# Kernel optimization log

Hardware: AMD Instinct MI355X
Metric: run time of the kernel (lower is better)

The kernel has to match this reference:

```python
import jax, jax.numpy as jnp
import numpy as np

TIME = 10  # interpolation factor, hardcoded in the torch module


def _interpolation(poly, time=TIME):
    # poly: [B, M, 2] -> [B, M*time, 2]
    poly_roll = jnp.roll(poly, shift=1, axis=1)
    step = jnp.arange(time, dtype=poly.dtype) / time  # [time]
    # interp[b, m, t, c] = poly[b,m,c]*step[t] + roll[b,m,c]*(1-step[t])
    interp = (poly[:, :, None, :] * step[None, None, :, None]
              + poly_roll[:, :, None, :] * (1.0 - step)[None, None, :, None])
    B, M = poly.shape[0], poly.shape[1]
    return interp.reshape(B, M * time, 2)


def _compute_distance(pred_poly, gt_poly):
    # pred: [B, N, 2], gt: [B, G, 2] -> sq dist [B, G, N]
    diff = pred_poly[:, None, :, :] - gt_poly[:, :, None, :]
    return jnp.sum(diff * diff, axis=3)


def setup_inputs() -> dict:
    key = jax.random.key(0)
    k1, k2, k3 = jax.random.split(key, 3)
    B, N, M = 1024, 128, 128
    return {
        "ini_pred_poly": jax.random.normal(k1, (B, N, 2), dtype=jnp.float32),
        "pred_polys_": jax.random.normal(k2, (B, N, 2), dtype=jnp.float32),
        "gt_polys": jax.random.normal(k3, (B, M, 2), dtype=jnp.float32),
        "keyPointsMask": jnp.ones((B, M), dtype=jnp.float32),
    }


def reference(ini_pred_poly, pred_polys_, gt_polys, keyPointsMask):
    # ---- lossPred2NearestGt ----
    gt_interp = _interpolation(gt_polys)                     # [B, M*T, 2]
    dist_pg = _compute_distance(ini_pred_poly, gt_interp)    # [B, M*T, N]
    index_gt = jnp.argmin(dist_pg, axis=1)                   # [B, N]
    nearest_gt = jnp.take_along_axis(gt_interp, index_gt[:, :, None], axis=1)  # [B, N, 2]
    loss_pred2gt = jnp.mean(jnp.abs(pred_polys_ - nearest_gt))  # l1, mean reduction

    # ---- lossGt2NearestPred ----
    dist_gp = _compute_distance(ini_pred_poly, gt_polys)     # [B, M, N]
    index_pred = jnp.argmin(dist_gp, axis=2)                 # [B, M]
    nearest_pred = jnp.take_along_axis(pred_polys_, index_pred[:, :, None], axis=1)  # [B, M, 2]
    loss_gt2pred = jnp.abs(nearest_pred - gt_polys)          # [B, M, 2], reduction='none'

    mask = keyPointsMask[:, :, None] * jnp.ones((1, 1, 2), dtype=keyPointsMask.dtype)  # [B, M, 2]
    loss_set2set = jnp.sum(loss_gt2pred * mask) / (jnp.sum(mask) + 1.0) + loss_pred2gt
    return loss_set2set / 2.0
```

## Files before the change

### kernel.cpp

```cpp
#include <hip/hip_runtime.h>

constexpr int Bn = 1024;
constexpr int Nn = 128;
constexpr int Mn = 128;


__global__ __launch_bounds__(256) void dm_main(
    const float2* __restrict__ ini,
    const float2* __restrict__ pred,
    const float2* __restrict__ gt,
    const float*  __restrict__ kpm,
    float4* __restrict__ part)
{
    __shared__ float4 s_segA[Mn];
    __shared__ float2 s_segB[Mn];
    __shared__ float2 s_ini[Nn];
    __shared__ float2 s_pred[Nn];
    __shared__ float2 s_gt[Mn];
    __shared__ float  s_red[3][4];

    const int b   = blockIdx.x;
    const int tid = threadIdx.x;

    if (tid < Mn) {
        const float2 cur = gt[b*Mn + tid];
        const float2 prv = gt[b*Mn + ((tid + Mn - 1) & (Mn - 1))];
        const float ex = cur.x - prv.x, ey = cur.y - prv.y;
        const float ee = fmaxf(fmaf(ex, ex, ey*ey), 1e-30f);
        const float nr = -10.0f * __builtin_amdgcn_rcpf(ee);
        s_segA[tid] = make_float4(prv.x, prv.y, ex, ey);
        s_segB[tid] = make_float2(ee, nr);
        s_gt[tid]   = cur;
        s_ini[tid]  = ini[b*Nn + tid];
        s_pred[tid] = pred[b*Nn + tid];
    }
    __syncthreads();

    const int lane_s = tid & 1;
    const int n      = tid >> 1;
    const int base   = lane_s * 64;

    const float2 p = s_ini[n];
    float best = 3.4e38f; int bm = 0; float bs = 0.f;
    #pragma unroll 8
    for (int i = 0; i < 64; ++i) {
        const int m = base + i;
        const float4 A  = s_segA[m];
        const float2 Bv = s_segB[m];
        const float fx = A.x - p.x, fy = A.y - p.y;
        const float fe = fmaf(fx, A.z, fy*A.w);
        const float ff = fmaf(fx, fx, fy*fy);
        float tv = fe * Bv.y;
        tv = fminf(fmaxf(rintf(tv), 0.f), 9.f);
        const float sp = tv * 0.1f;
        const float d  = fmaf(sp, fmaf(sp, Bv.x, fe + fe), ff);
        if (d < best) { best = d; bm = m; bs = sp; }
    }
    {
        const float od = __shfl_xor(best, 1);
        const int   om = __shfl_xor(bm, 1);
        const float os = __shfl_xor(bs, 1);
        if (od < best || (od == best && om < bm)) { best = od; bm = om; bs = os; }
    }
    float sum_p2g = 0.f;
    if (lane_s == 0) {
        const float4 A = s_segA[bm];
        const float ngx = fmaf(bs, A.z, A.x);
        const float ngy = fmaf(bs, A.w, A.y);
        const float2 pr = s_pred[n];
        sum_p2g = fabsf(pr.x - ngx) + fabsf(pr.y - ngy);
    }

    const float2 g = s_gt[n];
    float best2 = 3.4e38f; int ni = 0;
    #pragma unroll 8
    for (int i = 0; i < 64; ++i) {
        const int j = base + i;
        const float2 q = s_ini[j];
        const float dx = q.x - g.x, dy = q.y - g.y;
        const float d = fmaf(dx, dx, dy*dy);
        if (d < best2) { best2 = d; ni = j; }
    }
    {
        const float od = __shfl_xor(best2, 1);
        const int   oi = __shfl_xor(ni, 1);
        if (od < best2 || (od == best2 && oi < ni)) { best2 = od; ni = oi; }
    }
    float sum_g2p = 0.f, sum_m = 0.f;
    if (lane_s == 0) {
        const float  w   = kpm[b*Mn + n];
        const float2 np_ = s_pred[ni];
        sum_g2p = w * (fabsf(np_.x - g.x) + fabsf(np_.y - g.y));
        sum_m   = 2.0f * w;
    }

    #pragma unroll
    for (int off = 32; off > 0; off >>= 1) {
        sum_p2g += __shfl_down(sum_p2g, off);
        sum_g2p += __shfl_down(sum_g2p, off);
        sum_m   += __shfl_down(sum_m,   off);
    }
    const int wv = tid >> 6;
    if ((tid & 63) == 0) { s_red[0][wv] = sum_p2g; s_red[1][wv] = sum_g2p; s_red[2][wv] = sum_m; }
    __syncthreads();
    if (tid == 0) {
        part[b] = make_float4(s_red[0][0] + s_red[0][1] + s_red[0][2] + s_red[0][3],
                              s_red[1][0] + s_red[1][1] + s_red[1][2] + s_red[1][3],
                              s_red[2][0] + s_red[2][1] + s_red[2][2] + s_red[2][3], 0.f);
    }
}

__global__ __launch_bounds__(1024) void dm_final(const float4* __restrict__ part,
                                                 float* __restrict__ out)
{
    __shared__ float s_red[3][16];
    const int tid = threadIdx.x;
    const float4 v = part[tid];
    float a = v.x, c = v.y, m = v.z;
    #pragma unroll
    for (int off = 32; off > 0; off >>= 1) {
        a += __shfl_down(a, off); c += __shfl_down(c, off); m += __shfl_down(m, off);
    }
    const int wv = tid >> 6;
    if ((tid & 63) == 0) { s_red[0][wv] = a; s_red[1][wv] = c; s_red[2][wv] = m; }
    __syncthreads();
    if (tid == 0) {
        float A = 0.f, C = 0.f, M = 0.f;
        #pragma unroll
        for (int i = 0; i < 16; ++i) { A += s_red[0][i]; C += s_red[1][i]; M += s_red[2][i]; }
        out[0] = (C / (M + 1.0f) + A * (1.0f / 262144.0f)) * 0.5f;
    }
}

extern "C" void kernel_launch(void* const* d_in, const int* in_sizes, int n_in,
                              void* d_out, int out_size, void* d_ws, size_t ws_size,
                              hipStream_t stream)
{
    const float2* ini  = (const float2*)d_in[0];
    const float2* pred = (const float2*)d_in[1];
    const float2* gt   = (const float2*)d_in[2];
    const float*  kpm  = (const float*)d_in[3];
    float*  out  = (float*)d_out;
    float4* part = (float4*)d_ws;

    dm_main<<<Bn, 256, 0, stream>>>(ini, pred, gt, kpm, part);
    dm_final<<<1, 1024, 0, stream>>>(part, out);
}
```

Before: 73.31 us.

## Split each batch across two blocks and pack argmin into sortable keys

```diff
diff --git a/kernel.cpp b/kernel.cpp
--- a/kernel.cpp
+++ b/kernel.cpp
@@ -19,7 +19,8 @@
     __shared__ float2 s_gt[Mn];
     __shared__ float  s_red[3][4];
 
-    const int b   = blockIdx.x;
+    const int b   = blockIdx.x >> 1;
+    const int h   = blockIdx.x & 1;
     const int tid = threadIdx.x;
 
     if (tid < Mn) {
@@ -27,69 +28,68 @@
         const float2 prv = gt[b*Mn + ((tid + Mn - 1) & (Mn - 1))];
         const float ex = cur.x - prv.x, ey = cur.y - prv.y;
         const float ee = fmaxf(fmaf(ex, ex, ey*ey), 1e-30f);
-        const float nr = -10.0f * __builtin_amdgcn_rcpf(ee);
         s_segA[tid] = make_float4(prv.x, prv.y, ex, ey);
-        s_segB[tid] = make_float2(ee, nr);
+        s_segB[tid] = make_float2(ee, -10.0f * __builtin_amdgcn_rcpf(ee));
         s_gt[tid]   = cur;
         s_ini[tid]  = ini[b*Nn + tid];
         s_pred[tid] = pred[b*Nn + tid];
     }
     __syncthreads();
 
-    const int lane_s = tid & 1;
-    const int n      = tid >> 1;
-    const int base   = lane_s * 64;
+    const int p    = tid >> 2;
+    const int q    = tid & 3;
+    const int n    = h*64 + p;
+    const int base = q*32;
 
-    const float2 p = s_ini[n];
-    float best = 3.4e38f; int bm = 0; float bs = 0.f;
+    const float2 P = s_ini[n];
+    unsigned bestA = 0xFFFFFFFFu;
     #pragma unroll 8
-    for (int i = 0; i < 64; ++i) {
+    for (int i = 0; i < 32; ++i) {
         const int m = base + i;
         const float4 A  = s_segA[m];
         const float2 Bv = s_segB[m];
-        const float fx = A.x - p.x, fy = A.y - p.y;
+        const float fx = A.x - P.x, fy = A.y - P.y;
         const float fe = fmaf(fx, A.z, fy*A.w);
         const float ff = fmaf(fx, fx, fy*fy);
-        float tv = fe * Bv.y;
-        tv = fminf(fmaxf(rintf(tv), 0.f), 9.f);
-        const float sp = tv * 0.1f;
-        const float d  = fmaf(sp, fmaf(sp, Bv.x, fe + fe), ff);
-        if (d < best) { best = d; bm = m; bs = sp; }
+        const float sp = 0.1f * __builtin_amdgcn_fmed3f(rintf(fe*Bv.y), 0.f, 9.f);
+        const float d  = fmaxf(fmaf(sp, fmaf(sp, Bv.x, fe + fe), ff), 0.f);
+        bestA = min(bestA, (__float_as_uint(d) & 0xFFFFFF80u) | (unsigned)m);
     }
-    {
-        const float od = __shfl_xor(best, 1);
-        const int   om = __shfl_xor(bm, 1);
-        const float os = __shfl_xor(bs, 1);
-        if (od < best || (od == best && om < bm)) { best = od; bm = om; bs = os; }
-    }
+    bestA = min(bestA, (unsigned)__shfl_xor((int)bestA, 1));
+    bestA = min(bestA, (unsigned)__shfl_xor((int)bestA, 2));
+
     float sum_p2g = 0.f;
-    if (lane_s == 0) {
-        const float4 A = s_segA[bm];
-        const float ngx = fmaf(bs, A.z, A.x);
-        const float ngy = fmaf(bs, A.w, A.y);
+    if (q == 0) {
+        const int bm = bestA & 127;
+        const float4 A  = s_segA[bm];
+        const float2 Bv = s_segB[bm];
+        const float fx = A.x - P.x, fy = A.y - P.y;
+        const float fe = fmaf(fx, A.z, fy*A.w);
+        const float sp = 0.1f * __builtin_amdgcn_fmed3f(rintf(fe*Bv.y), 0.f, 9.f);
+        const float ngx = fmaf(sp, A.z, A.x);
+        const float ngy = fmaf(sp, A.w, A.y);
         const float2 pr = s_pred[n];
         sum_p2g = fabsf(pr.x - ngx) + fabsf(pr.y - ngy);
     }
 
     const float2 g = s_gt[n];
-    float best2 = 3.4e38f; int ni = 0;
+    unsigned bestB = 0xFFFFFFFFu;
     #pragma unroll 8
-    for (int i = 0; i < 64; ++i) {
+    for (int i = 0; i < 32; ++i) {
         const int j = base + i;
-        const float2 q = s_ini[j];
-        const float dx = q.x - g.x, dy = q.y - g.y;
-        const float d = fmaf(dx, dx, dy*dy);
-        if (d < best2) { best2 = d; ni = j; }
+        const float2 Qp = s_ini[j];
+        const float dx = Qp.x - g.x, dy = Qp.y - g.y;
+        const float d  = fmaf(dx, dx, dy*dy);
+        bestB = min(bestB, (__float_as_uint(d) & 0xFFFFFF80u) | (unsigned)j);
     }
-    {
-        const float od = __shfl_xor(best2, 1);
-        const int   oi = __shfl_xor(ni, 1);
-        if (od < best2 || (od == best2 && oi < ni)) { best2 = od; ni = oi; }
-    }
+    bestB = min(bestB, (unsigned)__shfl_xor((int)bestB, 1));
+    bestB = min(bestB, (unsigned)__shfl_xor((int)bestB, 2));
+
     float sum_g2p = 0.f, sum_m = 0.f;
-    if (lane_s == 0) {
-        const float  w   = kpm[b*Mn + n];
-        const float2 np_ = s_pred[ni];
+    if (q == 0) {
+        const int   ni_ = bestB & 127;
+        const float w   = kpm[b*Mn + n];
+        const float2 np_ = s_pred[ni_];
         sum_g2p = w * (fabsf(np_.x - g.x) + fabsf(np_.y - g.y));
         sum_m   = 2.0f * w;
     }
@@ -104,9 +104,10 @@
     if ((tid & 63) == 0) { s_red[0][wv] = sum_p2g; s_red[1][wv] = sum_g2p; s_red[2][wv] = sum_m; }
     __syncthreads();
     if (tid == 0) {
-        part[b] = make_float4(s_red[0][0] + s_red[0][1] + s_red[0][2] + s_red[0][3],
-                              s_red[1][0] + s_red[1][1] + s_red[1][2] + s_red[1][3],
-                              s_red[2][0] + s_red[2][1] + s_red[2][2] + s_red[2][3], 0.f);
+        part[blockIdx.x] = make_float4(
+            s_red[0][0] + s_red[0][1] + s_red[0][2] + s_red[0][3],
+            s_red[1][0] + s_red[1][1] + s_red[1][2] + s_red[1][3],
+            s_red[2][0] + s_red[2][1] + s_red[2][2] + s_red[2][3], 0.f);
     }
 }
 
@@ -115,8 +116,9 @@
 {
     __shared__ float s_red[3][16];
     const int tid = threadIdx.x;
-    const float4 v = part[tid];
-    float a = v.x, c = v.y, m = v.z;
+    const float4 v0 = part[tid];
+    const float4 v1 = part[tid + 1024];
+    float a = v0.x + v1.x, c = v0.y + v1.y, m = v0.z + v1.z;
     #pragma unroll
     for (int off = 32; off > 0; off >>= 1) {
         a += __shfl_down(a, off); c += __shfl_down(c, off); m += __shfl_down(m, off);
@@ -143,6 +145,6 @@
     float*  out  = (float*)d_out;
     float4* part = (float4*)d_ws;
 
-    dm_main<<<Bn, 256, 0, stream>>>(ini, pred, gt, kpm, part);
+    dm_main<<<2*Bn, 256, 0, stream>>>(ini, pred, gt, kpm, part);
     dm_final<<<1, 1024, 0, stream>>>(part, out);
 }
```

Measured after the change: 80.02 us. +9.1%, slower.

## Precompute segment table in separate kernel and use packed argmin keys

Applied to the files above, without the earlier changes.

```diff
diff --git a/kernel.cpp b/kernel.cpp
--- a/kernel.cpp
+++ b/kernel.cpp
@@ -1,99 +1,75 @@
 #include <hip/hip_runtime.h>
 
 constexpr int Bn = 1024;
-constexpr int Nn = 128;
 constexpr int Mn = 128;
 
 
-__global__ __launch_bounds__(256) void dm_main(
+__global__ __launch_bounds__(256) void dm_pre(
+    const float2* __restrict__ ini,
+    const float2* __restrict__ gt,
+    float4* __restrict__ seg)
+{
+    const int idx = blockIdx.x * 256 + threadIdx.x;
+    const int b = idx >> 7, m = idx & 127;
+    const float2 cur = gt[idx];
+    const float2 prv = gt[(b << 7) | ((m + 127) & 127)];
+    const float2 ii  = ini[idx];
+    const float ex = cur.x - prv.x, ey = cur.y - prv.y;
+    const float ee = fmaxf(fmaf(ex, ex, ey * ey), 1e-30f);
+    const float nr = -10.0f * __builtin_amdgcn_rcpf(ee);
+    seg[2*idx]     = make_float4(prv.x, prv.y, ex, ey);
+    seg[2*idx + 1] = make_float4(ee, nr, ii.x, ii.y);
+}
+
+__global__ __launch_bounds__(128) void dm_main(
     const float2* __restrict__ ini,
     const float2* __restrict__ pred,
     const float2* __restrict__ gt,
     const float*  __restrict__ kpm,
+    const float4* __restrict__ seg,
     float4* __restrict__ part)
 {
-    __shared__ float4 s_segA[Mn];
-    __shared__ float2 s_segB[Mn];
-    __shared__ float2 s_ini[Nn];
-    __shared__ float2 s_pred[Nn];
-    __shared__ float2 s_gt[Mn];
-    __shared__ float  s_red[3][4];
+    const int b    = blockIdx.x;
+    const int tid  = threadIdx.x;
+    const int base = b * (2 * Mn);
 
-    const int b   = blockIdx.x;
-    const int tid = threadIdx.x;
+    const float2 P = ini[b*Mn + tid];
+    const float2 g = gt [b*Mn + tid];
 
-    if (tid < Mn) {
-        const float2 cur = gt[b*Mn + tid];
-        const float2 prv = gt[b*Mn + ((tid + Mn - 1) & (Mn - 1))];
-        const float ex = cur.x - prv.x, ey = cur.y - prv.y;
-        const float ee = fmaxf(fmaf(ex, ex, ey*ey), 1e-30f);
-        const float nr = -10.0f * __builtin_amdgcn_rcpf(ee);
-        s_segA[tid] = make_float4(prv.x, prv.y, ex, ey);
-        s_segB[tid] = make_float2(ee, nr);
-        s_gt[tid]   = cur;
-        s_ini[tid]  = ini[b*Nn + tid];
-        s_pred[tid] = pred[b*Nn + tid];
-    }
-    __syncthreads();
-
-    const int lane_s = tid & 1;
-    const int n      = tid >> 1;
-    const int base   = lane_s * 64;
-
-    const float2 p = s_ini[n];
-    float best = 3.4e38f; int bm = 0; float bs = 0.f;
+    unsigned bestA = 0xFFFFFFFFu, bestB = 0xFFFFFFFFu;
     #pragma unroll 8
-    for (int i = 0; i < 64; ++i) {
-        const int m = base + i;
-        const float4 A  = s_segA[m];
-        const float2 Bv = s_segB[m];
-        const float fx = A.x - p.x, fy = A.y - p.y;
-        const float fe = fmaf(fx, A.z, fy*A.w);
+    for (int m = 0; m < Mn; ++m) {
+        const float4 A1 = seg[base + 2*m];
+        const float4 A2 = seg[base + 2*m + 1];
+        const float fx = A1.x - P.x, fy = A1.y - P.y;
+        const float fe = fmaf(fx, A1.z, fy*A1.w);
         const float ff = fmaf(fx, fx, fy*fy);
-        float tv = fe * Bv.y;
-        tv = fminf(fmaxf(rintf(tv), 0.f), 9.f);
-        const float sp = tv * 0.1f;
-        const float d  = fmaf(sp, fmaf(sp, Bv.x, fe + fe), ff);
-        if (d < best) { best = d; bm = m; bs = sp; }
-    }
-    {
-        const float od = __shfl_xor(best, 1);
-        const int   om = __shfl_xor(bm, 1);
-        const float os = __shfl_xor(bs, 1);
-        if (od < best || (od == best && om < bm)) { best = od; bm = om; bs = os; }
-    }
-    float sum_p2g = 0.f;
-    if (lane_s == 0) {
-        const float4 A = s_segA[bm];
-        const float ngx = fmaf(bs, A.z, A.x);
-        const float ngy = fmaf(bs, A.w, A.y);
-        const float2 pr = s_pred[n];
-        sum_p2g = fabsf(pr.x - ngx) + fabsf(pr.y - ngy);
+        const float sp = 0.1f * __builtin_amdgcn_fmed3f(rintf(fe*A2.y), 0.f, 9.f);
+        const float d  = fmaxf(fmaf(sp, fmaf(sp, A2.x, fe + fe), ff), 0.f);
+        bestA = min(bestA, (__float_as_uint(d) & 0xFFFFFF80u) | (unsigned)m);
+        const float dx = A2.z - g.x, dy = A2.w - g.y;
+        const float d2 = fmaf(dx, dx, dy*dy);
+        bestB = min(bestB, (__float_as_uint(d2) & 0xFFFFFF80u) | (unsigned)m);
     }
 
-    const float2 g = s_gt[n];
-    float best2 = 3.4e38f; int ni = 0;
-    #pragma unroll 8
-    for (int i = 0; i < 64; ++i) {
-        const int j = base + i;
-        const float2 q = s_ini[j];
-        const float dx = q.x - g.x, dy = q.y - g.y;
-        const float d = fmaf(dx, dx, dy*dy);
-        if (d < best2) { best2 = d; ni = j; }
-    }
-    {
-        const float od = __shfl_xor(best2, 1);
-        const int   oi = __shfl_xor(ni, 1);
-        if (od < best2 || (od == best2 && oi < ni)) { best2 = od; ni = oi; }
-    }
-    float sum_g2p = 0.f, sum_m = 0.f;
-    if (lane_s == 0) {
-        const float  w   = kpm[b*Mn + n];
-        const float2 np_ = s_pred[ni];
-        sum_g2p = w * (fabsf(np_.x - g.x) + fabsf(np_.y - g.y));
-        sum_m   = 2.0f * w;
-    }
+    const int bm = bestA & 127;
+    const float4 R1 = seg[base + 2*bm];
+    const float4 R2 = seg[base + 2*bm + 1];
+    const float fx = R1.x - P.x, fy = R1.y - P.y;
+    const float fe = fmaf(fx, R1.z, fy*R1.w);
+    const float sp = 0.1f * __builtin_amdgcn_fmed3f(rintf(fe*R2.y), 0.f, 9.f);
+    const float ngx = fmaf(sp, R1.z, R1.x);
+    const float ngy = fmaf(sp, R1.w, R1.y);
+    const float2 pr = pred[b*Mn + tid];
+    float sum_p2g = fabsf(pr.x - ngx) + fabsf(pr.y - ngy);
 
+    const int   ni_ = bestB & 127;
+    const float2 np_ = pred[b*Mn + ni_];
+    const float  w   = kpm[b*Mn + tid];
+    float sum_g2p = w * (fabsf(np_.x - g.x) + fabsf(np_.y - g.y));
+    float sum_m   = 2.0f * w;
+
+    __shared__ float s_red[3][2];
     #pragma unroll
     for (int off = 32; off > 0; off >>= 1) {
         sum_p2g += __shfl_down(sum_p2g, off);
@@ -104,9 +80,9 @@
     if ((tid & 63) == 0) { s_red[0][wv] = sum_p2g; s_red[1][wv] = sum_g2p; s_red[2][wv] = sum_m; }
     __syncthreads();
     if (tid == 0) {
-        part[b] = make_float4(s_red[0][0] + s_red[0][1] + s_red[0][2] + s_red[0][3],
-                              s_red[1][0] + s_red[1][1] + s_red[1][2] + s_red[1][3],
-                              s_red[2][0] + s_red[2][1] + s_red[2][2] + s_red[2][3], 0.f);
+        part[b] = make_float4(s_red[0][0] + s_red[0][1],
+                              s_red[1][0] + s_red[1][1],
+                              s_red[2][0] + s_red[2][1], 0.f);
     }
 }
 
@@ -140,9 +116,12 @@
     const float2* pred = (const float2*)d_in[1];
     const float2* gt   = (const float2*)d_in[2];
     const float*  kpm  = (const float*)d_in[3];
-    float*  out  = (float*)d_out;
-    float4* part = (float4*)d_ws;
+    float* out = (float*)d_out;
 
-    dm_main<<<Bn, 256, 0, stream>>>(ini, pred, gt, kpm, part);
+    float4* seg  = (float4*)d_ws;
+    float4* part = seg + Bn * Mn * 2;
+
+    dm_pre <<<Bn * Mn / 256, 256, 0, stream>>>(ini, gt, seg);
+    dm_main<<<Bn, 128, 0, stream>>>(ini, pred, gt, kpm, seg, part);
     dm_final<<<1, 1024, 0, stream>>>(part, out);
 }
```

Measured after the change: 77.54 us. 1.06x slower.
